# Kernel tuning notes

Hardware: AMD Instinct MI355X
Metric: run time of the kernel (lower is better)

The kernel has to match this reference:

```python
import jax, jax.numpy as jnp
import numpy as np

N = 262144          # total neurons (num_neurons * batch_size)
S = 4194304         # total synapses (~16 per neuron)
L = 8               # delay ring-buffer length (steps)
DT = 1e-4
SLOPE = 4.0
T_NOW = 0.0
# uniform per-neuron params (original stores them via _full(const))
SOMA_C, SOMA_GL, SOMA_EL = 2e-10, 1e-8, -0.070
AIS_C, AIS_GL, AIS_EL = 1e-10, 1e-8, -0.070
V_T, DELTA_T, V_SPIKE, V_RESET = -0.050, 0.002, -0.030, -0.065
G_C = 5e-9
# uniform per-synapse params (tiled constants in connect())
G_MAX, E_REV, TAU_DECAY = 1e-9, 0.0, 0.005
A_PLUS, A_MINUS, TAU_PRE, TAU_POST = 0.01, 0.012, 0.020, 0.020
ETA_BCM, TAU_RATE, TAU_THETA = 1e-4, 0.100, 1.000
W_MIN, W_MAX = 0.0, 1.0


def setup_inputs() -> dict:
    key = jax.random.key(0)
    ks = jax.random.split(key, 14)
    return {
        "external_current": 2e-10 * jax.random.normal(ks[0], (N,), jnp.float32),
        "syn_w": jax.random.uniform(ks[1], (S,), jnp.float32),
        "V_soma": SOMA_EL + 0.005 * jax.random.normal(ks[2], (N,), jnp.float32),
        "V_ais": -0.050 + 0.030 * jax.random.normal(ks[3], (N,), jnp.float32),
        "refrac_until": jnp.full((N,), -1e9, jnp.float32),
        "syn_g": 0.5 * jax.random.uniform(ks[4], (S,), jnp.float32),
        "pre_trace": jax.random.uniform(ks[5], (S,), jnp.float32),
        "post_trace": jax.random.uniform(ks[6], (S,), jnp.float32),
        "r_pre": jax.random.uniform(ks[7], (S,), jnp.float32),
        "r_post": jax.random.uniform(ks[8], (S,), jnp.float32),
        "theta_m": jax.random.uniform(ks[9], (S,), jnp.float32),
        "g_incr_buffer": jnp.zeros((L, S), jnp.float32),
        "syn_pre_idx": jax.random.randint(ks[10], (S,), 0, N, jnp.int32),
        "syn_post_idx": jax.random.randint(ks[11], (S,), 0, N, jnp.int32),
        "delay_steps": jax.random.randint(ks[12], (S,), 1, L, jnp.int32),
        "buffer_idx": 0,
    }


def reference(external_current, syn_w, V_soma, V_ais, refrac_until, syn_g,
              pre_trace, post_trace, r_pre, r_post, theta_m,
              g_incr_buffer, syn_pre_idx, syn_post_idx, delay_steps, buffer_idx):
    n = V_soma.shape[0]
    # conductance-based synaptic current, gathered from post voltage, scattered to post neurons
    i_syn = syn_g * syn_w * G_MAX * (E_REV - V_soma[syn_post_idx])
    I_syn_total = jax.ops.segment_sum(i_syn, syn_post_idx, num_segments=n)
    # two-compartment step (explicit Euler): passive soma + AdEx AIS, coupled by g_c
    dvs = (DT / SOMA_C) * (-SOMA_GL * (V_soma - SOMA_EL) + external_current
                           + I_syn_total + G_C * (V_ais - V_soma))
    exp_term = AIS_GL * DELTA_T * jnp.exp(jnp.minimum((V_ais - V_T) / DELTA_T, 20.0))
    dva = (DT / AIS_C) * (-AIS_GL * (V_ais - AIS_EL) + exp_term + G_C * (V_soma - V_ais))
    V_soma_new = V_soma + dvs
    V_ais_new = jnp.where(T_NOW < refrac_until, V_RESET, V_ais + dva)
    # spike detection with sigmoid surrogate gradient
    hard = (V_ais_new >= V_SPIKE).astype(V_ais_new.dtype)
    soft = jax.nn.sigmoid(SLOPE * (V_ais_new - V_SPIKE))
    spikes = soft + jax.lax.stop_gradient(hard - soft)
    V_ais_out = jnp.where(hard > 0, V_RESET, V_ais_new)
    # conductance: exponential decay + delayed arrivals read from ring buffer slot
    arrivals = g_incr_buffer[buffer_idx]
    syn_g_new = syn_g * jnp.exp(-DT / TAU_DECAY) + arrivals
    pre_spk = spikes[syn_pre_idx]
    post_spk = spikes[syn_post_idx]
    # schedule this step's pre-spikes at per-synapse delay slots; clear consumed slot
    rows = (buffer_idx + delay_steps) % L
    buf_new = g_incr_buffer.at[buffer_idx].set(0.0).at[rows, jnp.arange(syn_w.shape[0])].add(pre_spk)
    # STDP eligibility traces
    pre_tr = pre_trace * jnp.exp(-DT / TAU_PRE) + pre_spk
    post_tr = post_trace * jnp.exp(-DT / TAU_POST) + post_spk
    dw_stdp = A_PLUS * pre_tr * post_spk - A_MINUS * post_tr * pre_spk
    # BCM low-pass rates and sliding threshold
    r_pre_n = r_pre * jnp.exp(-DT / TAU_RATE) + pre_spk
    r_post_n = r_post * jnp.exp(-DT / TAU_RATE) + post_spk
    theta_n = theta_m + (DT / TAU_THETA) * (r_post_n * r_post_n - theta_m)
    dw_bcm = ETA_BCM * r_pre_n * r_post_n * (r_post_n - theta_n)
    w_new = jnp.clip(syn_w + dw_stdp + dw_bcm, W_MIN, W_MAX)
    return (spikes, V_soma_new, V_ais_out, syn_g_new, w_new, buf_new)
```

## Files before the change

### kernel.cpp

```cpp
#include <hip/hip_runtime.h>
#include <math.h>

#define C_DT_OVER_SOMA  500000.0f
#define C_DT_OVER_AIS   1000000.0f
#define C_SOMA_GL       1e-8f
#define C_SOMA_EL       (-0.070f)
#define C_AIS_GL        1e-8f
#define C_AIS_EL        (-0.070f)
#define C_V_T           (-0.050f)
#define C_DELTA_T       0.002f
#define C_V_SPIKE       (-0.030f)
#define C_V_RESET       (-0.065f)
#define C_G_C           5e-9f
#define C_G_MAX         1e-9f
#define C_DECAY_G       0.9801986733067553f
#define C_DECAY_TR      0.9950124791926823f
#define C_DECAY_RATE    0.9990004998333751f
#define C_DT_TAU_THETA  1e-4f
#define C_A_PLUS        0.01f
#define C_A_MINUS       0.012f
#define C_ETA_BCM       1e-4f

#define TILE_BITS   15
#define TILE_SIZE   32768
#define TILE_MASK   (TILE_SIZE - 1)
#define NTILES      8
#define KCHUNK      32

__global__ void k_zero4(float4* __restrict__ p, int n4) {
    int i = blockIdx.x * blockDim.x + threadIdx.x;
    if (i < n4) p[i] = make_float4(0.f, 0.f, 0.f, 0.f);
}

__global__ void __launch_bounds__(512, 1)
k_scatter_tile(const float4* __restrict__ g4,
               const float4* __restrict__ w4,
               const int4*   __restrict__ post4,
               float*        __restrict__ partials,
               int S) {
    extern __shared__ float acc[];
    const int t = blockIdx.x & (NTILES - 1);
    const int k = blockIdx.x >> 3;

    for (int i = threadIdx.x; i < TILE_SIZE; i += blockDim.x)
        acc[i] = 0.0f;
    __syncthreads();

    const int cnt4  = (S / KCHUNK) / 4;
    const int base4 = k * cnt4;
    for (int j = threadIdx.x; j < cnt4; j += blockDim.x) {
        int4   p = post4[base4 + j];
        float4 g = g4[base4 + j];
        float4 w = w4[base4 + j];
        if ((p.x >> TILE_BITS) == t) atomicAdd(&acc[p.x & TILE_MASK], g.x * w.x);
        if ((p.y >> TILE_BITS) == t) atomicAdd(&acc[p.y & TILE_MASK], g.y * w.y);
        if ((p.z >> TILE_BITS) == t) atomicAdd(&acc[p.z & TILE_MASK], g.z * w.z);
        if ((p.w >> TILE_BITS) == t) atomicAdd(&acc[p.w & TILE_MASK], g.w * w.w);
    }
    __syncthreads();

    float4* dst = (float4*)(partials + (size_t)blockIdx.x * TILE_SIZE);
    const float4* src = (const float4*)acc;
    for (int i = threadIdx.x; i < TILE_SIZE / 4; i += blockDim.x)
        dst[i] = src[i];
}

template <bool FAST>
__global__ void k_neuron(const float* __restrict__ ext,
                         const float* __restrict__ Vs,
                         const float* __restrict__ Va,
                         const float* __restrict__ refrac,
                         const float* __restrict__ A,
                         float* __restrict__ spikes,
                         float* __restrict__ Vs_out,
                         float* __restrict__ Va_out,
                         int N) {
    int i = blockIdx.x * blockDim.x + threadIdx.x;
    if (i >= N) return;
    float acc = 0.0f;
    if (FAST) {
        const int t = i >> TILE_BITS;
        const int local = i & TILE_MASK;
        const float* base = A + ((size_t)t * KCHUNK) * TILE_SIZE + local;
        #pragma unroll
        for (int k = 0; k < KCHUNK; ++k) acc += base[(size_t)k * TILE_SIZE];
    } else {
        acc = A[i];
    }
    float vs = Vs[i];
    float va = Va[i];
    float I_syn = C_G_MAX * (0.0f - vs) * acc;
    float dvs = C_DT_OVER_SOMA * (-C_SOMA_GL * (vs - C_SOMA_EL) + ext[i]
                                  + I_syn + C_G_C * (va - vs));
    float xarg = fminf((va - C_V_T) / C_DELTA_T, 20.0f);
    float exp_term = C_AIS_GL * C_DELTA_T * expf(xarg);
    float dva = C_DT_OVER_AIS * (-C_AIS_GL * (va - C_AIS_EL) + exp_term
                                 + C_G_C * (vs - va));
    float vs_new = vs + dvs;
    float va_new = (0.0f < refrac[i]) ? C_V_RESET : (va + dva);
    float hard = (va_new >= C_V_SPIKE) ? 1.0f : 0.0f;
    float va_out = (hard > 0.0f) ? C_V_RESET : va_new;
    spikes[i] = hard;
    Vs_out[i] = vs_new;
    Va_out[i] = va_out;
}

__global__ void k_scatter_gw_dev(const float4* __restrict__ g4,
                                 const float4* __restrict__ w4,
                                 const int4*   __restrict__ post4,
                                 float*        __restrict__ A,
                                 int S4) {
    int t = blockIdx.x * blockDim.x + threadIdx.x;
    if (t >= S4) return;
    float4 g = g4[t];
    float4 w = w4[t];
    int4   p = post4[t];
    unsafeAtomicAdd(&A[p.x], g.x * w.x);
    unsafeAtomicAdd(&A[p.y], g.y * w.y);
    unsafeAtomicAdd(&A[p.z], g.z * w.z);
    unsafeAtomicAdd(&A[p.w], g.w * w.w);
}

__global__ void k_syn_update4(const float* __restrict__ syn_g,
                              const float* __restrict__ syn_w,
                              const float* __restrict__ pre_trace,
                              const float* __restrict__ post_trace,
                              const float* __restrict__ r_pre,
                              const float* __restrict__ r_post,
                              const float* __restrict__ theta_m,
                              const float* __restrict__ gbuf,
                              const int*   __restrict__ pre_idx,
                              const int*   __restrict__ post_idx,
                              const int*   __restrict__ delay,
                              const int*   __restrict__ bidx_p,
                              const float* __restrict__ spikes,
                              float* __restrict__ g_out,
                              float* __restrict__ w_out,
                              float* __restrict__ buf_out,
                              int S, int L) {
    int t = blockIdx.x * blockDim.x + threadIdx.x;
    int j = t * 4;
    if (j >= S) return;
    const int bidx = bidx_p[0];

    int4 pi = *(const int4*)(pre_idx + j);
    int4 qi = *(const int4*)(post_idx + j);
    int4 dl = *(const int4*)(delay + j);

    float pre[4], post[4];
    pre[0] = spikes[pi.x]; pre[1] = spikes[pi.y]; pre[2] = spikes[pi.z]; pre[3] = spikes[pi.w];
    post[0] = spikes[qi.x]; post[1] = spikes[qi.y]; post[2] = spikes[qi.z]; post[3] = spikes[qi.w];

    float4 g  = *(const float4*)(syn_g + j);
    float4 w  = *(const float4*)(syn_w + j);
    float4 pt = *(const float4*)(pre_trace + j);
    float4 qt = *(const float4*)(post_trace + j);
    float4 rp = *(const float4*)(r_pre + j);
    float4 rq = *(const float4*)(r_post + j);
    float4 th = *(const float4*)(theta_m + j);

    float wv[4]  = {w.x, w.y, w.z, w.w};
    float ptv[4] = {pt.x, pt.y, pt.z, pt.w};
    float qtv[4] = {qt.x, qt.y, qt.z, qt.w};
    float rpv[4] = {rp.x, rp.y, rp.z, rp.w};
    float rqv[4] = {rq.x, rq.y, rq.z, rq.w};
    float thv[4] = {th.x, th.y, th.z, th.w};
    float wo[4];
    #pragma unroll
    for (int k = 0; k < 4; ++k) {
        float ptr_n = ptv[k] * C_DECAY_TR + pre[k];
        float qtr_n = qtv[k] * C_DECAY_TR + post[k];
        float dw_stdp = C_A_PLUS * ptr_n * post[k] - C_A_MINUS * qtr_n * pre[k];
        float rpn = rpv[k] * C_DECAY_RATE + pre[k];
        float rqn = rqv[k] * C_DECAY_RATE + post[k];
        float thn = thv[k] + C_DT_TAU_THETA * (rqn * rqn - thv[k]);
        float dw_bcm = C_ETA_BCM * rpn * rqn * (rqn - thn);
        float wn = wv[k] + dw_stdp + dw_bcm;
        wo[k] = fminf(fmaxf(wn, 0.0f), 1.0f);
    }
    float4 wo4 = {wo[0], wo[1], wo[2], wo[3]};
    *(float4*)(w_out + j) = wo4;

    int row[4];
    row[0] = (bidx + dl.x) % L;
    row[1] = (bidx + dl.y) % L;
    row[2] = (bidx + dl.z) % L;
    row[3] = (bidx + dl.w) % L;
    float gv[4] = {g.x, g.y, g.z, g.w};
    for (int r = 0; r < L; ++r) {
        float4 v = *(const float4*)(gbuf + (size_t)r * (size_t)S + j);
        float vv[4] = {v.x, v.y, v.z, v.w};
        if (r == bidx) {
            float4 gn;
            gn.x = gv[0] * C_DECAY_G + vv[0];
            gn.y = gv[1] * C_DECAY_G + vv[1];
            gn.z = gv[2] * C_DECAY_G + vv[2];
            gn.w = gv[3] * C_DECAY_G + vv[3];
            *(float4*)(g_out + j) = gn;
            vv[0] = vv[1] = vv[2] = vv[3] = 0.0f;
        }
        #pragma unroll
        for (int k = 0; k < 4; ++k)
            if (r == row[k]) vv[k] += pre[k];
        float4 ov = {vv[0], vv[1], vv[2], vv[3]};
        *(float4*)(buf_out + (size_t)r * (size_t)S + j) = ov;
    }
}

extern "C" void kernel_launch(void* const* d_in, const int* in_sizes, int n_in,
                              void* d_out, int out_size, void* d_ws, size_t ws_size,
                              hipStream_t stream) {
    const int N = in_sizes[0];
    const int S = in_sizes[1];
    const int L = in_sizes[11] / S;

    const float* ext        = (const float*)d_in[0];
    const float* syn_w      = (const float*)d_in[1];
    const float* Vs         = (const float*)d_in[2];
    const float* Va         = (const float*)d_in[3];
    const float* refrac     = (const float*)d_in[4];
    const float* syn_g      = (const float*)d_in[5];
    const float* pre_trace  = (const float*)d_in[6];
    const float* post_trace = (const float*)d_in[7];
    const float* r_pre      = (const float*)d_in[8];
    const float* r_post     = (const float*)d_in[9];
    const float* theta_m    = (const float*)d_in[10];
    const float* gbuf       = (const float*)d_in[11];
    const int*   pre_idx    = (const int*)d_in[12];
    const int*   post_idx   = (const int*)d_in[13];
    const int*   delay      = (const int*)d_in[14];
    const int*   bidx       = (const int*)d_in[15];

    float* out     = (float*)d_out;
    float* spikes  = out;
    float* Vs_out  = out + (size_t)N;
    float* Va_out  = out + (size_t)2 * N;
    float* g_out   = out + (size_t)3 * N;
    float* w_out   = out + (size_t)3 * N + (size_t)S;
    float* buf_out = out + (size_t)3 * N + (size_t)2 * S;

    float* A = (float*)d_ws;

    const size_t need = (size_t)NTILES * KCHUNK * TILE_SIZE * sizeof(float);
    const bool fast = (N == NTILES * TILE_SIZE) &&
                      (S % (KCHUNK * 4) == 0) &&
                      (ws_size >= need);

    const int B = 256;
    if (fast) {
        k_scatter_tile<<<NTILES * KCHUNK, 512, TILE_SIZE * sizeof(float), stream>>>(
            (const float4*)syn_g, (const float4*)syn_w, (const int4*)post_idx, A, S);
        k_neuron<true><<<(N + B - 1) / B, B, 0, stream>>>(ext, Vs, Va, refrac, A,
                                                          spikes, Vs_out, Va_out, N);
    } else {
        const int S4 = S / 4;
        k_zero4<<<(N / 4 + B - 1) / B, B, 0, stream>>>((float4*)A, N / 4);
        k_scatter_gw_dev<<<(S4 + B - 1) / B, B, 0, stream>>>((const float4*)syn_g,
                                                             (const float4*)syn_w,
                                                             (const int4*)post_idx, A, S4);
        k_neuron<false><<<(N + B - 1) / B, B, 0, stream>>>(ext, Vs, Va, refrac, A,
                                                           spikes, Vs_out, Va_out, N);
    }
    const int T4 = (S + 3) / 4;
    k_syn_update4<<<(T4 + B - 1) / B, B, 0, stream>>>(syn_g, syn_w, pre_trace, post_trace,
                                                      r_pre, r_post, theta_m, gbuf,
                                                      pre_idx, post_idx, delay, bidx,
                                                      spikes, g_out, w_out, buf_out, S, L);
}
```

Baseline: 196.9 us.

## Split synapse update into plasticity and ring-buffer kernels with unrolled loads

Replaces the single fused synapse-update kernel with two kernels when L is 8. One handles STDP/BCM weight plasticity at 8 synapses per thread; the other handles conductance decay and the ring-buffer rewrite with L templated, so all eight row loads are issued up front and modulo becomes a mask. The aim is to raise memory-level parallelism and shorten per-thread register/latency chains in the bandwidth-bound synapse pass. In exchange, pre_idx is read twice and spikes are gathered twice, and there is an extra launch.

```diff
diff --git a/kernel.cpp b/kernel.cpp
--- a/kernel.cpp
+++ b/kernel.cpp
@@ -121,6 +121,123 @@
     unsafeAtomicAdd(&A[p.w], g.w * w.w);
 }
 
+__global__ void k_plast8(const float* __restrict__ syn_w,
+                         const float* __restrict__ pre_trace,
+                         const float* __restrict__ post_trace,
+                         const float* __restrict__ r_pre,
+                         const float* __restrict__ r_post,
+                         const float* __restrict__ theta_m,
+                         const int*   __restrict__ pre_idx,
+                         const int*   __restrict__ post_idx,
+                         const float* __restrict__ spikes,
+                         float* __restrict__ w_out,
+                         int S) {
+    int t = blockIdx.x * blockDim.x + threadIdx.x;
+    int j = t * 8;
+    if (j >= S) return;
+
+    int4 pi0 = *(const int4*)(pre_idx + j);
+    int4 pi1 = *(const int4*)(pre_idx + j + 4);
+    int4 qi0 = *(const int4*)(post_idx + j);
+    int4 qi1 = *(const int4*)(post_idx + j + 4);
+
+    float4 w0  = *(const float4*)(syn_w + j);
+    float4 w1  = *(const float4*)(syn_w + j + 4);
+    float4 pt0 = *(const float4*)(pre_trace + j);
+    float4 pt1 = *(const float4*)(pre_trace + j + 4);
+    float4 qt0 = *(const float4*)(post_trace + j);
+    float4 qt1 = *(const float4*)(post_trace + j + 4);
+    float4 rp0 = *(const float4*)(r_pre + j);
+    float4 rp1 = *(const float4*)(r_pre + j + 4);
+    float4 rq0 = *(const float4*)(r_post + j);
+    float4 rq1 = *(const float4*)(r_post + j + 4);
+    float4 th0 = *(const float4*)(theta_m + j);
+    float4 th1 = *(const float4*)(theta_m + j + 4);
+
+    float pre[8], post[8];
+    pre[0] = spikes[pi0.x]; pre[1] = spikes[pi0.y]; pre[2] = spikes[pi0.z]; pre[3] = spikes[pi0.w];
+    pre[4] = spikes[pi1.x]; pre[5] = spikes[pi1.y]; pre[6] = spikes[pi1.z]; pre[7] = spikes[pi1.w];
+    post[0] = spikes[qi0.x]; post[1] = spikes[qi0.y]; post[2] = spikes[qi0.z]; post[3] = spikes[qi0.w];
+    post[4] = spikes[qi1.x]; post[5] = spikes[qi1.y]; post[6] = spikes[qi1.z]; post[7] = spikes[qi1.w];
+
+    float wv[8]  = {w0.x, w0.y, w0.z, w0.w, w1.x, w1.y, w1.z, w1.w};
+    float ptv[8] = {pt0.x, pt0.y, pt0.z, pt0.w, pt1.x, pt1.y, pt1.z, pt1.w};
+    float qtv[8] = {qt0.x, qt0.y, qt0.z, qt0.w, qt1.x, qt1.y, qt1.z, qt1.w};
+    float rpv[8] = {rp0.x, rp0.y, rp0.z, rp0.w, rp1.x, rp1.y, rp1.z, rp1.w};
+    float rqv[8] = {rq0.x, rq0.y, rq0.z, rq0.w, rq1.x, rq1.y, rq1.z, rq1.w};
+    float thv[8] = {th0.x, th0.y, th0.z, th0.w, th1.x, th1.y, th1.z, th1.w};
+    float wo[8];
+    #pragma unroll
+    for (int k = 0; k < 8; ++k) {
+        float ptr_n = ptv[k] * C_DECAY_TR + pre[k];
+        float qtr_n = qtv[k] * C_DECAY_TR + post[k];
+        float dw_stdp = C_A_PLUS * ptr_n * post[k] - C_A_MINUS * qtr_n * pre[k];
+        float rpn = rpv[k] * C_DECAY_RATE + pre[k];
+        float rqn = rqv[k] * C_DECAY_RATE + post[k];
+        float thn = thv[k] + C_DT_TAU_THETA * (rqn * rqn - thv[k]);
+        float dw_bcm = C_ETA_BCM * rpn * rqn * (rqn - thn);
+        float wn = wv[k] + dw_stdp + dw_bcm;
+        wo[k] = fminf(fmaxf(wn, 0.0f), 1.0f);
+    }
+    float4 a = {wo[0], wo[1], wo[2], wo[3]};
+    float4 b = {wo[4], wo[5], wo[6], wo[7]};
+    *(float4*)(w_out + j)     = a;
+    *(float4*)(w_out + j + 4) = b;
+}
+
+template <int L>
+__global__ void k_ring4(const float* __restrict__ syn_g,
+                        const float* __restrict__ gbuf,
+                        const int*   __restrict__ delay,
+                        const int*   __restrict__ pre_idx,
+                        const float* __restrict__ spikes,
+                        const int*   __restrict__ bidx_p,
+                        float* __restrict__ g_out,
+                        float* __restrict__ buf_out,
+                        int S) {
+    int t = blockIdx.x * blockDim.x + threadIdx.x;
+    int j = t * 4;
+    if (j >= S) return;
+    const int bidx = bidx_p[0];
+
+    int4 dl = *(const int4*)(delay + j);
+    int4 pi = *(const int4*)(pre_idx + j);
+    float4 g = *(const float4*)(syn_g + j);
+
+    float4 rowv[L];
+    #pragma unroll
+    for (int r = 0; r < L; ++r)
+        rowv[r] = *(const float4*)(gbuf + (size_t)r * (size_t)S + j);
+
+    float pre[4];
+    pre[0] = spikes[pi.x]; pre[1] = spikes[pi.y]; pre[2] = spikes[pi.z]; pre[3] = spikes[pi.w];
+
+    int row[4];
+    row[0] = (bidx + dl.x) & (L - 1);
+    row[1] = (bidx + dl.y) & (L - 1);
+    row[2] = (bidx + dl.z) & (L - 1);
+    row[3] = (bidx + dl.w) & (L - 1);
+
+    #pragma unroll
+    for (int r = 0; r < L; ++r) {
+        float4 v = rowv[r];
+        if (r == bidx) {
+            float4 gn;
+            gn.x = g.x * C_DECAY_G + v.x;
+            gn.y = g.y * C_DECAY_G + v.y;
+            gn.z = g.z * C_DECAY_G + v.z;
+            gn.w = g.w * C_DECAY_G + v.w;
+            *(float4*)(g_out + j) = gn;
+            v.x = v.y = v.z = v.w = 0.0f;
+        }
+        if (r == row[0]) v.x += pre[0];
+        if (r == row[1]) v.y += pre[1];
+        if (r == row[2]) v.z += pre[2];
+        if (r == row[3]) v.w += pre[3];
+        *(float4*)(buf_out + (size_t)r * (size_t)S + j) = v;
+    }
+}
+
 __global__ void k_syn_update4(const float* __restrict__ syn_g,
                               const float* __restrict__ syn_w,
                               const float* __restrict__ pre_trace,
@@ -142,15 +259,12 @@
     int j = t * 4;
     if (j >= S) return;
     const int bidx = bidx_p[0];
-
     int4 pi = *(const int4*)(pre_idx + j);
     int4 qi = *(const int4*)(post_idx + j);
     int4 dl = *(const int4*)(delay + j);
-
     float pre[4], post[4];
     pre[0] = spikes[pi.x]; pre[1] = spikes[pi.y]; pre[2] = spikes[pi.z]; pre[3] = spikes[pi.w];
     post[0] = spikes[qi.x]; post[1] = spikes[qi.y]; post[2] = spikes[qi.z]; post[3] = spikes[qi.w];
-
     float4 g  = *(const float4*)(syn_g + j);
     float4 w  = *(const float4*)(syn_w + j);
     float4 pt = *(const float4*)(pre_trace + j);
@@ -158,7 +272,6 @@
     float4 rp = *(const float4*)(r_pre + j);
     float4 rq = *(const float4*)(r_post + j);
     float4 th = *(const float4*)(theta_m + j);
-
     float wv[4]  = {w.x, w.y, w.z, w.w};
     float ptv[4] = {pt.x, pt.y, pt.z, pt.w};
     float qtv[4] = {qt.x, qt.y, qt.z, qt.w};
@@ -180,7 +293,6 @@
     }
     float4 wo4 = {wo[0], wo[1], wo[2], wo[3]};
     *(float4*)(w_out + j) = wo4;
-
     int row[4];
     row[0] = (bidx + dl.x) % L;
     row[1] = (bidx + dl.y) % L;
@@ -242,12 +354,13 @@
     float* A = (float*)d_ws;
 
     const size_t need = (size_t)NTILES * KCHUNK * TILE_SIZE * sizeof(float);
-    const bool fast = (N == NTILES * TILE_SIZE) &&
-                      (S % (KCHUNK * 4) == 0) &&
-                      (ws_size >= need);
+    const bool fastScatter = (N == NTILES * TILE_SIZE) &&
+                             (S % (KCHUNK * 4) == 0) &&
+                             (ws_size >= need);
+    const bool fastSyn = (L == 8) && (S % 32 == 0);
 
     const int B = 256;
-    if (fast) {
+    if (fastScatter) {
         k_scatter_tile<<<NTILES * KCHUNK, 512, TILE_SIZE * sizeof(float), stream>>>(
             (const float4*)syn_g, (const float4*)syn_w, (const int4*)post_idx, A, S);
         k_neuron<true><<<(N + B - 1) / B, B, 0, stream>>>(ext, Vs, Va, refrac, A,
@@ -261,9 +374,21 @@
         k_neuron<false><<<(N + B - 1) / B, B, 0, stream>>>(ext, Vs, Va, refrac, A,
                                                            spikes, Vs_out, Va_out, N);
     }
-    const int T4 = (S + 3) / 4;
-    k_syn_update4<<<(T4 + B - 1) / B, B, 0, stream>>>(syn_g, syn_w, pre_trace, post_trace,
-                                                      r_pre, r_post, theta_m, gbuf,
-                                                      pre_idx, post_idx, delay, bidx,
-                                                      spikes, g_out, w_out, buf_out, S, L);
-}
+
+    if (fastSyn) {
+        const int T8 = S / 8;
+        k_plast8<<<(T8 + B - 1) / B, B, 0, stream>>>(syn_w, pre_trace, post_trace,
+                                                     r_pre, r_post, theta_m,
+                                                     pre_idx, post_idx, spikes,
+                                                     w_out, S);
+        const int T4 = S / 4;
+        k_ring4<8><<<(T4 + B - 1) / B, B, 0, stream>>>(syn_g, gbuf, delay, pre_idx,
+                                                       spikes, bidx, g_out, buf_out, S);
+    } else {
+        const int T4 = (S + 3) / 4;
+        k_syn_update4<<<(T4 + B - 1) / B, B, 0, stream>>>(syn_g, syn_w, pre_trace, post_trace,
+                                                          r_pre, r_post, theta_m, gbuf,
+                                                          pre_idx, post_idx, delay, bidx,
+                                                          spikes, g_out, w_out, buf_out, S, L);
+    }
+}
```

New measurement: 220.8 us. +12.1%, slower.
